# Performance work log

Measured on AMD Instinct MI355X. Metric: run time of the kernel, lower is better.

Reference implementation:

```python
import jax, jax.numpy as jnp
import numpy as np

B = 4096           # number of paths
N_STEPS = 4        # module hops per path (3 with tanh + final without)
E = 128            # embed_size
NUM_AUTHOR = 500000
NUM_MODULE = 64
OUT_DIM = 16       # classifier_output_dim


def setup_inputs() -> dict:
    key = jax.random.key(0)
    ks = jax.random.split(key, 7)
    author_ids = jax.random.randint(ks[0], (B,), 0, NUM_AUTHOR)
    module_ids = jax.random.randint(ks[1], (B, N_STEPS), 0, NUM_MODULE)
    # learned parameters (torch nn.Embedding / nn.Linear layout: W is [out, in])
    embed_table = jax.random.normal(ks[2], (NUM_AUTHOR, E), dtype=jnp.float32)
    W = jax.random.normal(ks[3], (NUM_MODULE, E, E), dtype=jnp.float32) * (1.0 / np.sqrt(E))
    b = jax.random.normal(ks[4], (NUM_MODULE, E), dtype=jnp.float32) * 0.01
    cls_W = jax.random.normal(ks[5], (OUT_DIM, E), dtype=jnp.float32) * (1.0 / np.sqrt(E))
    cls_b = jax.random.normal(ks[6], (OUT_DIM,), dtype=jnp.float32) * 0.01
    return {"author_ids": author_ids, "module_ids": module_ids,
            "embed_table": embed_table, "W": W, "b": b,
            "cls_W": cls_W, "cls_b": cls_b}


def reference(author_ids, module_ids, embed_table, W, b, cls_W, cls_b):
    # x = author embedding lookup (path[0])           [B, E]
    x = embed_table[author_ids]
    n_steps = module_ids.shape[1]
    # dynamically-selected Linear+tanh chain; final Linear has no tanh
    for i in range(n_steps):
        ids = module_ids[:, i]                        # [B]
        Wi = W[ids]                                   # [B, E, E] (out, in)
        bi = b[ids]                                   # [B, E]
        y = jnp.einsum('bi,boi->bo', x, Wi) + bi
        x = jnp.tanh(y) if i < n_steps - 1 else y
    # classifier: Linear(E -> OUT_DIM)
    return x @ cls_W.T + cls_b
```

## Files before the change

kernel.cpp:

```cpp
#include <hip/hip_runtime.h>

#define B_TOT   4096
#define NSTEPS  4
#define E       128
#define OUT_DIM 16
#define NMOD    64
#define KSPLIT  8
#define TILE    16

#define XBUF_BYTE  67584
#define WFRAG_BYTE 2164736

using frag8 = __attribute__((ext_vector_type(8))) short;
using f32x4 = __attribute__((ext_vector_type(4))) float;

__device__ __forceinline__ unsigned short f2bf(float x) {
    union { float f; unsigned u; } v; v.f = x;
    unsigned r = v.u + 0x7FFFu + ((v.u >> 16) & 1u);
    return (unsigned short)(r >> 16);
}
__device__ __forceinline__ float bf2f(unsigned short h) {
    union { unsigned u; float f; } v; v.u = ((unsigned)h) << 16;
    return v.f;
}
__device__ __forceinline__ unsigned pack2(unsigned short a, unsigned short b) {
    return (unsigned)a | ((unsigned)b << 16);
}
__device__ __forceinline__ frag8 u4frag(uint4 u) {
    union { uint4 u; frag8 f; } v; v.u = u; return v.f;
}
__device__ __forceinline__ float tanh_fast(float x) {
    return 1.0f - 2.0f / (__expf(2.0f * x) + 1.0f);
}

__global__ __launch_bounds__(1024) void prep_sort_kernel(
    const int* __restrict__ mids, const float* __restrict__ W, int* __restrict__ ws)
{
    const int t = threadIdx.x;
    if (blockIdx.x < NSTEPS) {
        const int s = blockIdx.x;
        __shared__ int h[NMOD];
        __shared__ int o[NMOD];
        if (t < NMOD) h[t] = 0;
        __syncthreads();
        for (int b = t; b < B_TOT; b += 1024)
            atomicAdd(&h[mids[b * NSTEPS + s]], 1);
        __syncthreads();
        if (t == 0) {
            int run = 0;
            for (int m = 0; m < NMOD; ++m) { o[m] = run; run += h[m]; }
        }
        __syncthreads();
        if (t < NMOD) {
            ws[s * NMOD + t]       = h[t];
            ws[256 + s * NMOD + t] = o[t];
            h[t] = o[t];
        }
        __syncthreads();
        int* perm = ws + 512 + s * B_TOT;
        for (int b = t; b < B_TOT; b += 1024) {
            const int m = mids[b * NSTEPS + s];
            const int p = atomicAdd(&h[m], 1);
            perm[p] = b;
        }
    } else {
        const int m = blockIdx.x - NSTEPS;
        uint4* __restrict__ wf = (uint4*)((char*)ws + WFRAG_BYTE);
        const f32x4* __restrict__ wg = (const f32x4*)(W + (size_t)m * E * E);
        #pragma unroll
        for (int i = 0; i < 2; ++i) {
            const int f  = i * 1024 + t;
            const int c  = f >> 4;
            const int ss = (f >> 2) & 3;
            const int g  = f & 3;
            const int fi = (c * E + ss * 32 + g * 8) >> 2;
            const f32x4 v0 = wg[fi];
            const f32x4 v1 = wg[fi + 1];
            const float xf[8] = {v0.x, v0.y, v0.z, v0.w, v1.x, v1.y, v1.z, v1.w};
            unsigned short hh[8], qq[8];
            #pragma unroll
            for (int j = 0; j < 8; ++j) {
                hh[j] = f2bf(xf[j]);
                qq[j] = f2bf(xf[j] - bf2f(hh[j]));
            }
            const uint4 H = { pack2(hh[0], hh[1]), pack2(hh[2], hh[3]),
                              pack2(hh[4], hh[5]), pack2(hh[6], hh[7]) };
            const uint4 L = { pack2(qq[0], qq[1]), pack2(qq[2], qq[3]),
                              pack2(qq[4], qq[5]), pack2(qq[6], qq[7]) };
            const int u = m * 4096 + ss * 512 + c * 4 + g;
            wf[u]        = H;
            wf[u + 2048] = L;
        }
    }
}

template <bool FIRST, bool LAST>
__global__ __launch_bounds__(256) void step_kernel(
    const int s,
    const int* __restrict__ ws,
    const int* __restrict__ author_ids,
    const float* __restrict__ embed,
    const float* __restrict__ bias,
    const float* __restrict__ cls_W,
    const float* __restrict__ cls_b,
    float* __restrict__ out)
{
    const int m = blockIdx.x >> 3;
    const int k = blockIdx.x & (KSPLIT - 1);
    const int cnt = ws[s * NMOD + m];
    const int off = ws[256 + s * NMOD + m];
    const int start = off + k * TILE;
    const int end   = off + cnt;
    if (start >= end) return;

    const int t  = threadIdx.x;
    const int w  = t >> 6;
    const int l  = t & 63;
    const int g  = l >> 4;
    const int r0 = l & 15;
    const int c0 = 32 * w + r0;
    const int c1 = c0 + 16;

    const int* __restrict__ perm = ws + 512 + s * B_TOT;
    unsigned* __restrict__ xbufP = (unsigned*)((char*)ws + XBUF_BYTE);
    const uint4* __restrict__ wf = (const uint4*)((char*)ws + WFRAG_BYTE) + m * 4096;

    const float b0 = bias[m * E + c0];
    const float b1 = bias[m * E + c1];

    __shared__ __align__(16) float Yl[LAST ? TILE * (E + 4) : 1];

    for (int base = start; base < end; base += KSPLIT * TILE) {
        const int nb = min(TILE, end - base);

        const bool rok = r0 < nb;
        const int pa = perm[min(base + r0, B_TOT - 1)];
        frag8 ahi[4], alo[4];
        if (FIRST) {
            const f32x4* __restrict__ src =
                (const f32x4*)(embed + (size_t)author_ids[pa] * E);
            #pragma unroll
            for (int ss = 0; ss < 4; ++ss) {
                f32x4 v0 = {0.f, 0.f, 0.f, 0.f}, v1 = {0.f, 0.f, 0.f, 0.f};
                if (rok) { v0 = src[8 * ss + 2 * g]; v1 = src[8 * ss + 2 * g + 1]; }
                const float xf[8] = {v0.x, v0.y, v0.z, v0.w, v1.x, v1.y, v1.z, v1.w};
                #pragma unroll
                for (int j = 0; j < 8; ++j) {
                    const unsigned short hh = f2bf(xf[j]);
                    ahi[ss][j] = (short)hh;
                    alo[ss][j] = (short)f2bf(xf[j] - bf2f(hh));
                }
            }
        } else {
            const uint4* __restrict__ src = (const uint4*)(xbufP + (size_t)pa * E);
            #pragma unroll
            for (int ss = 0; ss < 4; ++ss) {
                uint4 p0 = {0, 0, 0, 0}, p1 = {0, 0, 0, 0};
                if (rok) { p0 = src[8 * ss + 2 * g]; p1 = src[8 * ss + 2 * g + 1]; }
                const unsigned pv[8] = {p0.x, p0.y, p0.z, p0.w, p1.x, p1.y, p1.z, p1.w};
                #pragma unroll
                for (int j = 0; j < 8; ++j) {
                    ahi[ss][j] = (short)(pv[j] >> 16);
                    alo[ss][j] = (short)(pv[j] & 0xFFFFu);
                }
            }
        }

        f32x4 acc0 = {0.f, 0.f, 0.f, 0.f};
        f32x4 acc1 = {0.f, 0.f, 0.f, 0.f};
        #pragma unroll
        for (int ss = 0; ss < 4; ++ss) {
            const int u0 = ss * 512 + c0 * 4 + g;
            const int u1 = ss * 512 + c1 * 4 + g;
            const frag8 bh0 = u4frag(wf[u0]);
            const frag8 bq0 = u4frag(wf[u0 + 2048]);
            const frag8 bh1 = u4frag(wf[u1]);
            const frag8 bq1 = u4frag(wf[u1 + 2048]);
            acc0 = __builtin_amdgcn_mfma_f32_16x16x32_bf16(ahi[ss], bh0, acc0, 0, 0, 0);
            acc0 = __builtin_amdgcn_mfma_f32_16x16x32_bf16(alo[ss], bh0, acc0, 0, 0, 0);
            acc0 = __builtin_amdgcn_mfma_f32_16x16x32_bf16(ahi[ss], bq0, acc0, 0, 0, 0);
            acc1 = __builtin_amdgcn_mfma_f32_16x16x32_bf16(ahi[ss], bh1, acc1, 0, 0, 0);
            acc1 = __builtin_amdgcn_mfma_f32_16x16x32_bf16(alo[ss], bh1, acc1, 0, 0, 0);
            acc1 = __builtin_amdgcn_mfma_f32_16x16x32_bf16(ahi[ss], bq1, acc1, 0, 0, 0);
        }

        if (!LAST) {
            #pragma unroll
            for (int r = 0; r < 4; ++r) {
                const int row = 4 * g + r;
                if (row < nb) {
                    const int rb = perm[base + row];
                    const float y0 = tanh_fast(acc0[r] + b0);
                    const float y1 = tanh_fast(acc1[r] + b1);
                    const unsigned short h0 = f2bf(y0);
                    const unsigned short h1 = f2bf(y1);
                    unsigned* __restrict__ dst = xbufP + (size_t)rb * E;
                    dst[c0] = pack2(f2bf(y0 - bf2f(h0)), h0);
                    dst[c1] = pack2(f2bf(y1 - bf2f(h1)), h1);
                }
            }
        } else {
            #pragma unroll
            for (int r = 0; r < 4; ++r) {
                const int row = 4 * g + r;
                Yl[row * (E + 4) + c0] = acc0[r] + b0;
                Yl[row * (E + 4) + c1] = acc1[r] + b1;
            }
            __syncthreads();
            const int row = t >> 4, j = t & 15;
            if (row < nb) {
                const f32x4* __restrict__ cw = (const f32x4*)(cls_W + j * E);
                float a2 = cls_b[j];
                #pragma unroll 8
                for (int jj = 0; jj < 32; ++jj) {
                    const f32x4 y4 = *(const f32x4*)&Yl[row * (E + 4) + jj * 4];
                    const f32x4 w4 = cw[jj];
                    a2 += y4.x * w4.x + y4.y * w4.y + y4.z * w4.z + y4.w * w4.w;
                }
                out[(size_t)perm[base + row] * OUT_DIM + j] = a2;
            }
            __syncthreads();
        }
    }
}

extern "C" void kernel_launch(void* const* d_in, const int* in_sizes, int n_in,
                              void* d_out, int out_size, void* d_ws, size_t ws_size,
                              hipStream_t stream) {
    const int*   author_ids = (const int*)d_in[0];
    const int*   module_ids = (const int*)d_in[1];
    const float* embed      = (const float*)d_in[2];
    const float* W          = (const float*)d_in[3];
    const float* bias       = (const float*)d_in[4];
    const float* cls_W      = (const float*)d_in[5];
    const float* cls_b      = (const float*)d_in[6];
    float* out = (float*)d_out;
    int*   wsI = (int*)d_ws;

    prep_sort_kernel<<<NSTEPS + NMOD, 1024, 0, stream>>>(module_ids, W, wsI);

    const dim3 g(NMOD * KSPLIT), blk(256);
    step_kernel<true,  false><<<g, blk, 0, stream>>>(0, wsI, author_ids, embed, bias, cls_W, cls_b, out);
    step_kernel<false, false><<<g, blk, 0, stream>>>(1, wsI, author_ids, embed, bias, cls_W, cls_b, out);
    step_kernel<false, false><<<g, blk, 0, stream>>>(2, wsI, author_ids, embed, bias, cls_W, cls_b, out);
    step_kernel<false, true ><<<g, blk, 0, stream>>>(3, wsI, author_ids, embed, bias, cls_W, cls_b, out);
}
```

Measured before the change: 50.14 us.

## Fuse prep and all step kernels into one cooperative kernel with grid syncs

Replaces the sort/prep kernel and four per-step launches with a single cooperative kernel of 256 blocks that uses grid-wide syncs between phases. Weight fragment conversion is spread across all non-sort blocks, the prefix scan uses wave shuffles, and KSPLIT drops to 4 so each module gets 4 blocks. This removes four launch gaps, at the cost of grid-barrier overhead and fewer blocks per module, which means more tiles processed serially per block.

```diff
diff --git a/kernel.cpp b/kernel.cpp
--- a/kernel.cpp
+++ b/kernel.cpp
@@ -1,12 +1,16 @@
 #include <hip/hip_runtime.h>
+#include <hip/hip_cooperative_groups.h>
+
+namespace cg = cooperative_groups;
 
 #define B_TOT   4096
 #define NSTEPS  4
 #define E       128
 #define OUT_DIM 16
 #define NMOD    64
-#define KSPLIT  8
+#define KSPLIT  4
 #define TILE    16
+#define GRID    256
 
 #define XBUF_BYTE  67584
 #define WFRAG_BYTE 2164736
@@ -33,22 +37,40 @@
     return 1.0f - 2.0f / (__expf(2.0f * x) + 1.0f);
 }
 
-__global__ __launch_bounds__(1024) void prep_sort_kernel(
-    const int* __restrict__ mids, const float* __restrict__ W, int* __restrict__ ws)
+__global__ __launch_bounds__(256) void fused_all(
+    const int* __restrict__ mids,
+    const int* __restrict__ author_ids,
+    const float* __restrict__ embed,
+    const float* __restrict__ W,
+    const float* __restrict__ bias,
+    const float* __restrict__ cls_W,
+    const float* __restrict__ cls_b,
+    float* __restrict__ out,
+    int* __restrict__ ws)
 {
-    const int t = threadIdx.x;
-    if (blockIdx.x < NSTEPS) {
-        const int s = blockIdx.x;
-        __shared__ int h[NMOD];
-        __shared__ int o[NMOD];
+    const int bid = blockIdx.x;
+    const int t   = threadIdx.x;
+
+    __shared__ __align__(16) float Yl[TILE * (E + 4)];
+    int* h = (int*)Yl;
+    int* o = h + NMOD;
+
+    if (bid < NSTEPS) {
+        const int s = bid;
         if (t < NMOD) h[t] = 0;
         __syncthreads();
-        for (int b = t; b < B_TOT; b += 1024)
+        for (int b = t; b < B_TOT; b += 256)
             atomicAdd(&h[mids[b * NSTEPS + s]], 1);
         __syncthreads();
-        if (t == 0) {
-            int run = 0;
-            for (int m = 0; m < NMOD; ++m) { o[m] = run; run += h[m]; }
+        if (t < NMOD) {
+            const int v = h[t];
+            int inc = v;
+            #pragma unroll
+            for (int d = 1; d < NMOD; d <<= 1) {
+                const int nv = __shfl_up(inc, d, 64);
+                if (t >= d) inc += nv;
+            }
+            o[t] = inc - v;
         }
         __syncthreads();
         if (t < NMOD) {
@@ -58,24 +80,22 @@
         }
         __syncthreads();
         int* perm = ws + 512 + s * B_TOT;
-        for (int b = t; b < B_TOT; b += 1024) {
+        for (int b = t; b < B_TOT; b += 256) {
             const int m = mids[b * NSTEPS + s];
-            const int p = atomicAdd(&h[m], 1);
-            perm[p] = b;
+            perm[atomicAdd(&h[m], 1)] = b;
         }
     } else {
-        const int m = blockIdx.x - NSTEPS;
         uint4* __restrict__ wf = (uint4*)((char*)ws + WFRAG_BYTE);
-        const f32x4* __restrict__ wg = (const f32x4*)(W + (size_t)m * E * E);
-        #pragma unroll
-        for (int i = 0; i < 2; ++i) {
-            const int f  = i * 1024 + t;
-            const int c  = f >> 4;
-            const int ss = (f >> 2) & 3;
-            const int g  = f & 3;
-            const int fi = (c * E + ss * 32 + g * 8) >> 2;
-            const f32x4 v0 = wg[fi];
-            const f32x4 v1 = wg[fi + 1];
+        for (int q = (bid - NSTEPS) * 256 + t; q < NMOD * 2048; q += (GRID - NSTEPS) * 256) {
+            const int m  = q >> 11;
+            const int u  = q & 2047;
+            const int ss = u >> 9;
+            const int c  = (u >> 2) & 127;
+            const int g  = u & 3;
+            const f32x4* __restrict__ src =
+                (const f32x4*)(W + (size_t)m * E * E + c * E + ss * 32 + g * 8);
+            const f32x4 v0 = src[0];
+            const f32x4 v1 = src[1];
             const float xf[8] = {v0.x, v0.y, v0.z, v0.w, v1.x, v1.y, v1.z, v1.w};
             unsigned short hh[8], qq[8];
             #pragma unroll
@@ -87,33 +107,15 @@
                               pack2(hh[4], hh[5]), pack2(hh[6], hh[7]) };
             const uint4 L = { pack2(qq[0], qq[1]), pack2(qq[2], qq[3]),
                               pack2(qq[4], qq[5]), pack2(qq[6], qq[7]) };
-            const int u = m * 4096 + ss * 512 + c * 4 + g;
-            wf[u]        = H;
-            wf[u + 2048] = L;
+            wf[m * 4096 + u]        = H;
+            wf[m * 4096 + u + 2048] = L;
         }
     }
-}
-
-template <bool FIRST, bool LAST>
-__global__ __launch_bounds__(256) void step_kernel(
-    const int s,
-    const int* __restrict__ ws,
-    const int* __restrict__ author_ids,
-    const float* __restrict__ embed,
-    const float* __restrict__ bias,
-    const float* __restrict__ cls_W,
-    const float* __restrict__ cls_b,
-    float* __restrict__ out)
-{
-    const int m = blockIdx.x >> 3;
-    const int k = blockIdx.x & (KSPLIT - 1);
-    const int cnt = ws[s * NMOD + m];
-    const int off = ws[256 + s * NMOD + m];
-    const int start = off + k * TILE;
-    const int end   = off + cnt;
-    if (start >= end) return;
-
-    const int t  = threadIdx.x;
+
+    cg::this_grid().sync();
+
+    const int m = bid & (NMOD - 1);
+    const int k = bid >> 6;
     const int w  = t >> 6;
     const int l  = t & 63;
     const int g  = l >> 4;
@@ -121,106 +123,113 @@
     const int c0 = 32 * w + r0;
     const int c1 = c0 + 16;
 
-    const int* __restrict__ perm = ws + 512 + s * B_TOT;
     unsigned* __restrict__ xbufP = (unsigned*)((char*)ws + XBUF_BYTE);
     const uint4* __restrict__ wf = (const uint4*)((char*)ws + WFRAG_BYTE) + m * 4096;
-
     const float b0 = bias[m * E + c0];
     const float b1 = bias[m * E + c1];
 
-    __shared__ __align__(16) float Yl[LAST ? TILE * (E + 4) : 1];
-
-    for (int base = start; base < end; base += KSPLIT * TILE) {
-        const int nb = min(TILE, end - base);
-
-        const bool rok = r0 < nb;
-        const int pa = perm[min(base + r0, B_TOT - 1)];
-        frag8 ahi[4], alo[4];
-        if (FIRST) {
-            const f32x4* __restrict__ src =
-                (const f32x4*)(embed + (size_t)author_ids[pa] * E);
+    for (int s = 0; s < NSTEPS; ++s) {
+        const bool FIRST = (s == 0);
+        const bool LAST  = (s == NSTEPS - 1);
+        const int cnt = ws[s * NMOD + m];
+        const int off = ws[256 + s * NMOD + m];
+        const int end = off + cnt;
+        const int* __restrict__ perm = ws + 512 + s * B_TOT;
+
+        for (int base = off + k * TILE; base < end; base += KSPLIT * TILE) {
+            const int nb = min(TILE, end - base);
+            const bool rok = r0 < nb;
+            const int pa = perm[min(base + r0, B_TOT - 1)];
+
+            frag8 ahi[4], alo[4];
+            if (FIRST) {
+                const f32x4* __restrict__ src =
+                    (const f32x4*)(embed + (size_t)author_ids[pa] * E);
+                #pragma unroll
+                for (int ss = 0; ss < 4; ++ss) {
+                    f32x4 v0 = {0.f, 0.f, 0.f, 0.f}, v1 = {0.f, 0.f, 0.f, 0.f};
+                    if (rok) { v0 = src[8 * ss + 2 * g]; v1 = src[8 * ss + 2 * g + 1]; }
+                    const float xf[8] = {v0.x, v0.y, v0.z, v0.w, v1.x, v1.y, v1.z, v1.w};
+                    #pragma unroll
+                    for (int j = 0; j < 8; ++j) {
+                        const unsigned short hh = f2bf(xf[j]);
+                        ahi[ss][j] = (short)hh;
+                        alo[ss][j] = (short)f2bf(xf[j] - bf2f(hh));
+                    }
+                }
+            } else {
+                const uint4* __restrict__ src = (const uint4*)(xbufP + (size_t)pa * E);
+                #pragma unroll
+                for (int ss = 0; ss < 4; ++ss) {
+                    uint4 p0 = {0, 0, 0, 0}, p1 = {0, 0, 0, 0};
+                    if (rok) { p0 = src[8 * ss + 2 * g]; p1 = src[8 * ss + 2 * g + 1]; }
+                    const unsigned pv[8] = {p0.x, p0.y, p0.z, p0.w, p1.x, p1.y, p1.z, p1.w};
+                    #pragma unroll
+                    for (int j = 0; j < 8; ++j) {
+                        ahi[ss][j] = (short)(pv[j] >> 16);
+                        alo[ss][j] = (short)(pv[j] & 0xFFFFu);
+                    }
+                }
+            }
+
+            f32x4 acc0 = {0.f, 0.f, 0.f, 0.f};
+            f32x4 acc1 = {0.f, 0.f, 0.f, 0.f};
             #pragma unroll
             for (int ss = 0; ss < 4; ++ss) {
-                f32x4 v0 = {0.f, 0.f, 0.f, 0.f}, v1 = {0.f, 0.f, 0.f, 0.f};
-                if (rok) { v0 = src[8 * ss + 2 * g]; v1 = src[8 * ss + 2 * g + 1]; }
-                const float xf[8] = {v0.x, v0.y, v0.z, v0.w, v1.x, v1.y, v1.z, v1.w};
-                #pragma unroll
-                for (int j = 0; j < 8; ++j) {
-                    const unsigned short hh = f2bf(xf[j]);
-                    ahi[ss][j] = (short)hh;
-                    alo[ss][j] = (short)f2bf(xf[j] - bf2f(hh));
-                }
-            }
-        } else {
-            const uint4* __restrict__ src = (const uint4*)(xbufP + (size_t)pa * E);
-            #pragma unroll
-            for (int ss = 0; ss < 4; ++ss) {
-                uint4 p0 = {0, 0, 0, 0}, p1 = {0, 0, 0, 0};
-                if (rok) { p0 = src[8 * ss + 2 * g]; p1 = src[8 * ss + 2 * g + 1]; }
-                const unsigned pv[8] = {p0.x, p0.y, p0.z, p0.w, p1.x, p1.y, p1.z, p1.w};
-                #pragma unroll
-                for (int j = 0; j < 8; ++j) {
-                    ahi[ss][j] = (short)(pv[j] >> 16);
-                    alo[ss][j] = (short)(pv[j] & 0xFFFFu);
-                }
-            }
-        }
-
-        f32x4 acc0 = {0.f, 0.f, 0.f, 0.f};
-        f32x4 acc1 = {0.f, 0.f, 0.f, 0.f};
-        #pragma unroll
-        for (int ss = 0; ss < 4; ++ss) {
-            const int u0 = ss * 512 + c0 * 4 + g;
-            const int u1 = ss * 512 + c1 * 4 + g;
-            const frag8 bh0 = u4frag(wf[u0]);
-            const frag8 bq0 = u4frag(wf[u0 + 2048]);
-            const frag8 bh1 = u4frag(wf[u1]);
-            const frag8 bq1 = u4frag(wf[u1 + 2048]);
-            acc0 = __builtin_amdgcn_mfma_f32_16x16x32_bf16(ahi[ss], bh0, acc0, 0, 0, 0);
-            acc0 = __builtin_amdgcn_mfma_f32_16x16x32_bf16(alo[ss], bh0, acc0, 0, 0, 0);
-            acc0 = __builtin_amdgcn_mfma_f32_16x16x32_bf16(ahi[ss], bq0, acc0, 0, 0, 0);
-            acc1 = __builtin_amdgcn_mfma_f32_16x16x32_bf16(ahi[ss], bh1, acc1, 0, 0, 0);
-            acc1 = __builtin_amdgcn_mfma_f32_16x16x32_bf16(alo[ss], bh1, acc1, 0, 0, 0);
-            acc1 = __builtin_amdgcn_mfma_f32_16x16x32_bf16(ahi[ss], bq1, acc1, 0, 0, 0);
-        }
-
-        if (!LAST) {
-            #pragma unroll
-            for (int r = 0; r < 4; ++r) {
-                const int row = 4 * g + r;
+                const int u0 = ss * 512 + c0 * 4 + g;
+                const int u1 = ss * 512 + c1 * 4 + g;
+                const frag8 bh0 = u4frag(wf[u0]);
+                const frag8 bq0 = u4frag(wf[u0 + 2048]);
+                const frag8 bh1 = u4frag(wf[u1]);
+                const frag8 bq1 = u4frag(wf[u1 + 2048]);
+                acc0 = __builtin_amdgcn_mfma_f32_16x16x32_bf16(ahi[ss], bh0, acc0, 0, 0, 0);
+                acc0 = __builtin_amdgcn_mfma_f32_16x16x32_bf16(alo[ss], bh0, acc0, 0, 0, 0);
+                acc0 = __builtin_amdgcn_mfma_f32_16x16x32_bf16(ahi[ss], bq0, acc0, 0, 0, 0);
+                acc1 = __builtin_amdgcn_mfma_f32_16x16x32_bf16(ahi[ss], bh1, acc1, 0, 0, 0);
+                acc1 = __builtin_amdgcn_mfma_f32_16x16x32_bf16(alo[ss], bh1, acc1, 0, 0, 0);
+                acc1 = __builtin_amdgcn_mfma_f32_16x16x32_bf16(ahi[ss], bq1, acc1, 0, 0, 0);
+            }
+
+            if (!LAST) {
+                #pragma unroll
+                for (int r = 0; r < 4; ++r) {
+                    const int row = 4 * g + r;
+                    if (row < nb) {
+                        const int rb = perm[base + row];
+                        const float y0 = tanh_fast(acc0[r] + b0);
+                        const float y1 = tanh_fast(acc1[r] + b1);
+                        const unsigned short h0 = f2bf(y0);
+                        const unsigned short h1 = f2bf(y1);
+                        unsigned* __restrict__ dst = xbufP + (size_t)rb * E;
+                        dst[c0] = pack2(f2bf(y0 - bf2f(h0)), h0);
+                        dst[c1] = pack2(f2bf(y1 - bf2f(h1)), h1);
+                    }
+                }
+            } else {
+                #pragma unroll
+                for (int r = 0; r < 4; ++r) {
+                    const int row = 4 * g + r;
+                    Yl[row * (E + 4) + c0] = acc0[r] + b0;
+                    Yl[row * (E + 4) + c1] = acc1[r] + b1;
+                }
+                __syncthreads();
+                const int row = t >> 4, j = t & 15;
                 if (row < nb) {
-                    const int rb = perm[base + row];
-                    const float y0 = tanh_fast(acc0[r] + b0);
-                    const float y1 = tanh_fast(acc1[r] + b1);
-                    const unsigned short h0 = f2bf(y0);
-                    const unsigned short h1 = f2bf(y1);
-                    unsigned* __restrict__ dst = xbufP + (size_t)rb * E;
-                    dst[c0] = pack2(f2bf(y0 - bf2f(h0)), h0);
-                    dst[c1] = pack2(f2bf(y1 - bf2f(h1)), h1);
-                }
-            }
-        } else {
-            #pragma unroll
-            for (int r = 0; r < 4; ++r) {
-                const int row = 4 * g + r;
-                Yl[row * (E + 4) + c0] = acc0[r] + b0;
-                Yl[row * (E + 4) + c1] = acc1[r] + b1;
-            }
-            __syncthreads();
-            const int row = t >> 4, j = t & 15;
-            if (row < nb) {
-                const f32x4* __restrict__ cw = (const f32x4*)(cls_W + j * E);
-                float a2 = cls_b[j];
-                #pragma unroll 8
-                for (int jj = 0; jj < 32; ++jj) {
-                    const f32x4 y4 = *(const f32x4*)&Yl[row * (E + 4) + jj * 4];
-                    const f32x4 w4 = cw[jj];
-                    a2 += y4.x * w4.x + y4.y * w4.y + y4.z * w4.z + y4.w * w4.w;
-                }
-                out[(size_t)perm[base + row] * OUT_DIM + j] = a2;
-            }
-            __syncthreads();
-        }
+                    const f32x4* __restrict__ cw = (const f32x4*)(cls_W + j * E);
+                    float a2 = cls_b[j];
+                    #pragma unroll 8
+                    for (int jj = 0; jj < 32; ++jj) {
+                        const f32x4 y4 = *(const f32x4*)&Yl[row * (E + 4) + jj * 4];
+                        const f32x4 w4 = cw[jj];
+                        a2 += y4.x * w4.x + y4.y * w4.y + y4.z * w4.z + y4.w * w4.w;
+                    }
+                    out[(size_t)perm[base + row] * OUT_DIM + j] = a2;
+                }
+                __syncthreads();
+            }
+        }
+
+        if (s < NSTEPS - 1) cg::this_grid().sync();
     }
 }
 
@@ -237,11 +246,10 @@
     float* out = (float*)d_out;
     int*   wsI = (int*)d_ws;
 
-    prep_sort_kernel<<<NSTEPS + NMOD, 1024, 0, stream>>>(module_ids, W, wsI);
-
-    const dim3 g(NMOD * KSPLIT), blk(256);
-    step_kernel<true,  false><<<g, blk, 0, stream>>>(0, wsI, author_ids, embed, bias, cls_W, cls_b, out);
-    step_kernel<false, false><<<g, blk, 0, stream>>>(1, wsI, author_ids, embed, bias, cls_W, cls_b, out);
-    step_kernel<false, false><<<g, blk, 0, stream>>>(2, wsI, author_ids, embed, bias, cls_W, cls_b, out);
-    step_kernel<false, true ><<<g, blk, 0, stream>>>(3, wsI, author_ids, embed, bias, cls_W, cls_b, out);
-}
+    void* args[] = {
+        (void*)&module_ids, (void*)&author_ids, (void*)&embed, (void*)&W,
+        (void*)&bias, (void*)&cls_W, (void*)&cls_b, (void*)&out, (void*)&wsI
+    };
+    hipLaunchCooperativeKernel((void*)fused_all, dim3(GRID), dim3(256),
+                               args, 0, stream);
+}
```

Result: slower. 171.6 us (+242.3%).

## Switch to fp16 MFMA with split weights and rank-ordered activation buffers

Applied to the files above, without the earlier changes.

Replaces the three-pass bf16 hi/lo split MFMA with fp16 activations times fp16 hi+lo split weights, cutting MFMAs per tile from six to four and halving activation storage. Activations are written directly in the next step's sorted order via a rank table, so reads become contiguous. Author ids are pre-permuted in the prep kernel, and weight fragments are hoisted into registers before the early exit. The prefix sum now uses a wave shuffle scan instead of a serial loop. Activations are rounded to a single fp16, so precision drops and values risk overflow or underflow compared with the bf16 pair.

```diff
diff --git a/kernel.cpp b/kernel.cpp
--- a/kernel.cpp
+++ b/kernel.cpp
@@ -8,33 +8,25 @@
 #define KSPLIT  8
 #define TILE    16
 
-#define XBUF_BYTE  67584
-#define WFRAG_BYTE 2164736
-
-using frag8 = __attribute__((ext_vector_type(8))) short;
+#define PERM_I   512
+#define RANK_I   16896
+#define PERMA0_I 33280
+#define XB0_BYTE (1u << 20)
+#define XB1_BYTE (4u << 20)
+#define WF_BYTE  (8u << 20)
+
+typedef _Float16 f16;
+using f16x8 = __attribute__((ext_vector_type(8))) f16;
 using f32x4 = __attribute__((ext_vector_type(4))) float;
-
-__device__ __forceinline__ unsigned short f2bf(float x) {
-    union { float f; unsigned u; } v; v.f = x;
-    unsigned r = v.u + 0x7FFFu + ((v.u >> 16) & 1u);
-    return (unsigned short)(r >> 16);
-}
-__device__ __forceinline__ float bf2f(unsigned short h) {
-    union { unsigned u; float f; } v; v.u = ((unsigned)h) << 16;
-    return v.f;
-}
-__device__ __forceinline__ unsigned pack2(unsigned short a, unsigned short b) {
-    return (unsigned)a | ((unsigned)b << 16);
-}
-__device__ __forceinline__ frag8 u4frag(uint4 u) {
-    union { uint4 u; frag8 f; } v; v.u = u; return v.f;
-}
+union U4H8 { uint4 u; f16x8 h; };
+
 __device__ __forceinline__ float tanh_fast(float x) {
     return 1.0f - 2.0f / (__expf(2.0f * x) + 1.0f);
 }
 
-__global__ __launch_bounds__(1024) void prep_sort_kernel(
-    const int* __restrict__ mids, const float* __restrict__ W, int* __restrict__ ws)
+__global__ __launch_bounds__(1024) void prep_kernel(
+    const int* __restrict__ mids, const int* __restrict__ author_ids,
+    const float* __restrict__ W, int* __restrict__ ws)
 {
     const int t = threadIdx.x;
     if (blockIdx.x < NSTEPS) {
@@ -46,9 +38,15 @@
         for (int b = t; b < B_TOT; b += 1024)
             atomicAdd(&h[mids[b * NSTEPS + s]], 1);
         __syncthreads();
-        if (t == 0) {
-            int run = 0;
-            for (int m = 0; m < NMOD; ++m) { o[m] = run; run += h[m]; }
+        if (t < NMOD) {
+            const int v = h[t];
+            int inc = v;
+            #pragma unroll
+            for (int d = 1; d < NMOD; d <<= 1) {
+                const int nv = __shfl_up(inc, d, 64);
+                if (t >= d) inc += nv;
+            }
+            o[t] = inc - v;
         }
         __syncthreads();
         if (t < NMOD) {
@@ -57,39 +55,43 @@
             h[t] = o[t];
         }
         __syncthreads();
-        int* perm = ws + 512 + s * B_TOT;
+        int* __restrict__ perm = ws + PERM_I + s * B_TOT;
+        int* __restrict__ rank = ws + RANK_I + s * B_TOT;
         for (int b = t; b < B_TOT; b += 1024) {
             const int m = mids[b * NSTEPS + s];
             const int p = atomicAdd(&h[m], 1);
             perm[p] = b;
+            rank[b] = p;
+        }
+        if (s == 0) {
+            __syncthreads();
+            int* __restrict__ pa0 = ws + PERMA0_I;
+            for (int pos = t; pos < B_TOT; pos += 1024)
+                pa0[pos] = author_ids[perm[pos]];
         }
     } else {
         const int m = blockIdx.x - NSTEPS;
-        uint4* __restrict__ wf = (uint4*)((char*)ws + WFRAG_BYTE);
-        const f32x4* __restrict__ wg = (const f32x4*)(W + (size_t)m * E * E);
+        uint4* __restrict__ wf = (uint4*)((char*)ws + WF_BYTE) + m * 4096;
         #pragma unroll
         for (int i = 0; i < 2; ++i) {
-            const int f  = i * 1024 + t;
-            const int c  = f >> 4;
-            const int ss = (f >> 2) & 3;
-            const int g  = f & 3;
-            const int fi = (c * E + ss * 32 + g * 8) >> 2;
-            const f32x4 v0 = wg[fi];
-            const f32x4 v1 = wg[fi + 1];
+            const int u  = i * 1024 + t;
+            const int ss = u >> 9;
+            const int c  = (u >> 2) & 127;
+            const int g  = u & 3;
+            const f32x4* __restrict__ src =
+                (const f32x4*)(W + (size_t)m * E * E + c * E + ss * 32 + g * 8);
+            const f32x4 v0 = src[0];
+            const f32x4 v1 = src[1];
             const float xf[8] = {v0.x, v0.y, v0.z, v0.w, v1.x, v1.y, v1.z, v1.w};
-            unsigned short hh[8], qq[8];
+            U4H8 hi, lo;
             #pragma unroll
             for (int j = 0; j < 8; ++j) {
-                hh[j] = f2bf(xf[j]);
-                qq[j] = f2bf(xf[j] - bf2f(hh[j]));
-            }
-            const uint4 H = { pack2(hh[0], hh[1]), pack2(hh[2], hh[3]),
-                              pack2(hh[4], hh[5]), pack2(hh[6], hh[7]) };
-            const uint4 L = { pack2(qq[0], qq[1]), pack2(qq[2], qq[3]),
-                              pack2(qq[4], qq[5]), pack2(qq[6], qq[7]) };
-            const int u = m * 4096 + ss * 512 + c * 4 + g;
-            wf[u]        = H;
-            wf[u + 2048] = L;
+                const f16 hh = (f16)xf[j];
+                hi.h[j] = hh;
+                lo.h[j] = (f16)(xf[j] - (float)hh);
+            }
+            wf[u]        = hi.u;
+            wf[u + 2048] = lo.u;
         }
     }
 }
@@ -98,21 +100,17 @@
 __global__ __launch_bounds__(256) void step_kernel(
     const int s,
     const int* __restrict__ ws,
-    const int* __restrict__ author_ids,
     const float* __restrict__ embed,
     const float* __restrict__ bias,
     const float* __restrict__ cls_W,
     const float* __restrict__ cls_b,
+    const f16* __restrict__ Xin,
+    f16* __restrict__ Xout,
+    const int* __restrict__ rankN,
     float* __restrict__ out)
 {
     const int m = blockIdx.x >> 3;
     const int k = blockIdx.x & (KSPLIT - 1);
-    const int cnt = ws[s * NMOD + m];
-    const int off = ws[256 + s * NMOD + m];
-    const int start = off + k * TILE;
-    const int end   = off + cnt;
-    if (start >= end) return;
-
     const int t  = threadIdx.x;
     const int w  = t >> 6;
     const int l  = t & 63;
@@ -121,67 +119,66 @@
     const int c0 = 32 * w + r0;
     const int c1 = c0 + 16;
 
-    const int* __restrict__ perm = ws + 512 + s * B_TOT;
-    unsigned* __restrict__ xbufP = (unsigned*)((char*)ws + XBUF_BYTE);
-    const uint4* __restrict__ wf = (const uint4*)((char*)ws + WFRAG_BYTE) + m * 4096;
+    const uint4* __restrict__ wf = (const uint4*)((const char*)ws + WF_BYTE) + m * 4096;
+    U4H8 BH0[4], BL0[4], BH1[4], BL1[4];
+    #pragma unroll
+    for (int ss = 0; ss < 4; ++ss) {
+        const int u0 = ss * 512 + c0 * 4 + g;
+        const int u1 = ss * 512 + c1 * 4 + g;
+        BH0[ss].u = wf[u0];
+        BL0[ss].u = wf[u0 + 2048];
+        BH1[ss].u = wf[u1];
+        BL1[ss].u = wf[u1 + 2048];
+    }
+
+    const int cnt = ws[s * NMOD + m];
+    const int off = ws[256 + s * NMOD + m];
+    const int start = off + k * TILE;
+    const int end   = off + cnt;
+    if (start >= end) return;
 
     const float b0 = bias[m * E + c0];
     const float b1 = bias[m * E + c1];
+    const int* __restrict__ permS = ws + PERM_I + s * B_TOT;
+    const int* __restrict__ pa0   = ws + PERMA0_I;
 
     __shared__ __align__(16) float Yl[LAST ? TILE * (E + 4) : 1];
 
     for (int base = start; base < end; base += KSPLIT * TILE) {
         const int nb = min(TILE, end - base);
-
-        const bool rok = r0 < nb;
-        const int pa = perm[min(base + r0, B_TOT - 1)];
-        frag8 ahi[4], alo[4];
+        const int rr = min(base + r0, B_TOT - 1);
+
+        int dmap;
+        if (!LAST) dmap = rankN[permS[rr]];
+        else       dmap = permS[rr];
+
+        f16x8 A[4];
         if (FIRST) {
             const f32x4* __restrict__ src =
-                (const f32x4*)(embed + (size_t)author_ids[pa] * E);
+                (const f32x4*)(embed + (size_t)pa0[rr] * E);
             #pragma unroll
             for (int ss = 0; ss < 4; ++ss) {
-                f32x4 v0 = {0.f, 0.f, 0.f, 0.f}, v1 = {0.f, 0.f, 0.f, 0.f};
-                if (rok) { v0 = src[8 * ss + 2 * g]; v1 = src[8 * ss + 2 * g + 1]; }
+                const f32x4 v0 = src[ss * 8 + 2 * g];
+                const f32x4 v1 = src[ss * 8 + 2 * g + 1];
                 const float xf[8] = {v0.x, v0.y, v0.z, v0.w, v1.x, v1.y, v1.z, v1.w};
                 #pragma unroll
-                for (int j = 0; j < 8; ++j) {
-                    const unsigned short hh = f2bf(xf[j]);
-                    ahi[ss][j] = (short)hh;
-                    alo[ss][j] = (short)f2bf(xf[j] - bf2f(hh));
-                }
+                for (int j = 0; j < 8; ++j) A[ss][j] = (f16)xf[j];
             }
         } else {
-            const uint4* __restrict__ src = (const uint4*)(xbufP + (size_t)pa * E);
-            #pragma unroll
-            for (int ss = 0; ss < 4; ++ss) {
-                uint4 p0 = {0, 0, 0, 0}, p1 = {0, 0, 0, 0};
-                if (rok) { p0 = src[8 * ss + 2 * g]; p1 = src[8 * ss + 2 * g + 1]; }
-                const unsigned pv[8] = {p0.x, p0.y, p0.z, p0.w, p1.x, p1.y, p1.z, p1.w};
-                #pragma unroll
-                for (int j = 0; j < 8; ++j) {
-                    ahi[ss][j] = (short)(pv[j] >> 16);
-                    alo[ss][j] = (short)(pv[j] & 0xFFFFu);
-                }
-            }
+            const U4H8* __restrict__ src = (const U4H8*)(Xin + (size_t)rr * E);
+            #pragma unroll
+            for (int ss = 0; ss < 4; ++ss)
+                A[ss] = src[ss * 4 + g].h;
         }
 
         f32x4 acc0 = {0.f, 0.f, 0.f, 0.f};
         f32x4 acc1 = {0.f, 0.f, 0.f, 0.f};
         #pragma unroll
         for (int ss = 0; ss < 4; ++ss) {
-            const int u0 = ss * 512 + c0 * 4 + g;
-            const int u1 = ss * 512 + c1 * 4 + g;
-            const frag8 bh0 = u4frag(wf[u0]);
-            const frag8 bq0 = u4frag(wf[u0 + 2048]);
-            const frag8 bh1 = u4frag(wf[u1]);
-            const frag8 bq1 = u4frag(wf[u1 + 2048]);
-            acc0 = __builtin_amdgcn_mfma_f32_16x16x32_bf16(ahi[ss], bh0, acc0, 0, 0, 0);
-            acc0 = __builtin_amdgcn_mfma_f32_16x16x32_bf16(alo[ss], bh0, acc0, 0, 0, 0);
-            acc0 = __builtin_amdgcn_mfma_f32_16x16x32_bf16(ahi[ss], bq0, acc0, 0, 0, 0);
-            acc1 = __builtin_amdgcn_mfma_f32_16x16x32_bf16(ahi[ss], bh1, acc1, 0, 0, 0);
-            acc1 = __builtin_amdgcn_mfma_f32_16x16x32_bf16(alo[ss], bh1, acc1, 0, 0, 0);
-            acc1 = __builtin_amdgcn_mfma_f32_16x16x32_bf16(ahi[ss], bq1, acc1, 0, 0, 0);
+            acc0 = __builtin_amdgcn_mfma_f32_16x16x32_f16(A[ss], BH0[ss].h, acc0, 0, 0, 0);
+            acc1 = __builtin_amdgcn_mfma_f32_16x16x32_f16(A[ss], BH1[ss].h, acc1, 0, 0, 0);
+            acc0 = __builtin_amdgcn_mfma_f32_16x16x32_f16(A[ss], BL0[ss].h, acc0, 0, 0, 0);
+            acc1 = __builtin_amdgcn_mfma_f32_16x16x32_f16(A[ss], BL1[ss].h, acc1, 0, 0, 0);
         }
 
         if (!LAST) {
@@ -189,14 +186,10 @@
             for (int r = 0; r < 4; ++r) {
                 const int row = 4 * g + r;
                 if (row < nb) {
-                    const int rb = perm[base + row];
-                    const float y0 = tanh_fast(acc0[r] + b0);
-                    const float y1 = tanh_fast(acc1[r] + b1);
-                    const unsigned short h0 = f2bf(y0);
-                    const unsigned short h1 = f2bf(y1);
-                    unsigned* __restrict__ dst = xbufP + (size_t)rb * E;
-                    dst[c0] = pack2(f2bf(y0 - bf2f(h0)), h0);
-                    dst[c1] = pack2(f2bf(y1 - bf2f(h1)), h1);
+                    const int d = __shfl(dmap, row, 16);
+                    f16* __restrict__ dst = Xout + (size_t)d * E;
+                    dst[c0] = (f16)tanh_fast(acc0[r] + b0);
+                    dst[c1] = (f16)tanh_fast(acc1[r] + b1);
                 }
             }
         } else {
@@ -209,6 +202,7 @@
             __syncthreads();
             const int row = t >> 4, j = t & 15;
             if (row < nb) {
+                const int outb = __shfl(dmap, row, 16);
                 const f32x4* __restrict__ cw = (const f32x4*)(cls_W + j * E);
                 float a2 = cls_b[j];
                 #pragma unroll 8
@@ -217,7 +211,7 @@
                     const f32x4 w4 = cw[jj];
                     a2 += y4.x * w4.x + y4.y * w4.y + y4.z * w4.z + y4.w * w4.w;
                 }
-                out[(size_t)perm[base + row] * OUT_DIM + j] = a2;
+                out[(size_t)outb * OUT_DIM + j] = a2;
             }
             __syncthreads();
         }
@@ -236,12 +230,18 @@
     const float* cls_b      = (const float*)d_in[6];
     float* out = (float*)d_out;
     int*   wsI = (int*)d_ws;
-
-    prep_sort_kernel<<<NSTEPS + NMOD, 1024, 0, stream>>>(module_ids, W, wsI);
+    f16*   XB0 = (f16*)((char*)d_ws + XB0_BYTE);
+    f16*   XB1 = (f16*)((char*)d_ws + XB1_BYTE);
+
+    prep_kernel<<<NSTEPS + NMOD, 1024, 0, stream>>>(module_ids, author_ids, W, wsI);
 
     const dim3 g(NMOD * KSPLIT), blk(256);
-    step_kernel<true,  false><<<g, blk, 0, stream>>>(0, wsI, author_ids, embed, bias, cls_W, cls_b, out);
-    step_kernel<false, false><<<g, blk, 0, stream>>>(1, wsI, author_ids, embed, bias, cls_W, cls_b, out);
-    step_kernel<false, false><<<g, blk, 0, stream>>>(2, wsI, author_ids, embed, bias, cls_W, cls_b, out);
-    step_kernel<false, true ><<<g, blk, 0, stream>>>(3, wsI, author_ids, embed, bias, cls_W, cls_b, out);
-}
+    step_kernel<true,  false><<<g, blk, 0, stream>>>(0, wsI, embed, bias, cls_W, cls_b,
+        (const f16*)nullptr, XB0, wsI + RANK_I + 1 * B_TOT, out);
+    step_kernel<false, false><<<g, blk, 0, stream>>>(1, wsI, embed, bias, cls_W, cls_b,
+        XB0, XB1, wsI + RANK_I + 2 * B_TOT, out);
+    step_kernel<false, false><<<g, blk, 0, stream>>>(2, wsI, embed, bias, cls_W, cls_b,
+        XB1, XB0, wsI + RANK_I + 3 * B_TOT, out);
+    step_kernel<false, true ><<<g, blk, 0, stream>>>(3, wsI, embed, bias, cls_W, cls_b,
+        XB0, (f16*)nullptr, wsI, out);
+}
```

New measurement: 48.57 us. 3.1% less time.
